# Optimization experiments

Measured on AMD Instinct MI355X. Metric: run time of the kernel, lower is better.

The kernel has to match this reference:

```python
import jax, jax.numpy as jnp
import numpy as np
import math

# SS2D (VMamba v2) config
D_MODEL = 96
D_INNER = 192          # ssm_ratio * d_model (== d_expand, ssm_rank_ratio==ssm_ratio)
D_STATE = 16
DT_RANK = 6            # ceil(96/16)
K = 4                  # scan directions
D_CONV = 3
STEP = 2               # EfficientScan step_size
BATCH, H, W = 4, 64, 64  # H,W chosen even -> no padding branch
LN_EPS = 1e-5


def efficient_scan(x):
    # x: (B, C, H, W) with H,W divisible by STEP -> (B, 4, C, (H/2)*(W/2))
    Bn, C = x.shape[0], x.shape[1]
    xt = jnp.swapaxes(x, 2, 3)  # (B, C, W, H)
    xs0 = x[:, :, ::STEP, ::STEP].reshape(Bn, C, -1)
    xs1 = xt[:, :, ::STEP, 1::STEP].reshape(Bn, C, -1)
    xs2 = x[:, :, ::STEP, 1::STEP].reshape(Bn, C, -1)
    xs3 = xt[:, :, 1::STEP, 1::STEP].reshape(Bn, C, -1)
    return jnp.stack([xs0, xs1, xs2, xs3], axis=1)


def efficient_merge(ys, ori_h, ori_w):
    # ys: (B, 4, C, L') -> (B, C, ori_h*ori_w)
    Bn, _, C, _ = ys.shape
    Hs, Ws = ori_h // STEP, ori_w // STEP
    a = ys[:, 0].reshape(Bn, C, Hs, Ws)
    b = jnp.swapaxes(ys[:, 1].reshape(Bn, C, Ws, Hs), 2, 3)
    c = ys[:, 2].reshape(Bn, C, Hs, Ws)
    d = jnp.swapaxes(ys[:, 3].reshape(Bn, C, Ws, Hs), 2, 3)
    y = jnp.zeros((Bn, C, ori_h, ori_w), ys.dtype)
    y = y.at[:, :, ::STEP, ::STEP].set(a)
    y = y.at[:, :, 1::STEP, ::STEP].set(b)
    y = y.at[:, :, ::STEP, 1::STEP].set(c)
    y = y.at[:, :, 1::STEP, 1::STEP].set(d)
    return y.reshape(Bn, C, ori_h * ori_w)


def selective_scan(u, delta, A, Bs, Cs, D, delta_bias):
    # u, delta: (B, K*Dg, L); A: (K*Dg, N); Bs, Cs: (B, K, N, L); D, delta_bias: (K*Dg,)
    Bn, KD, L = u.shape
    N = A.shape[1]
    Dg = KD // K
    delta = jax.nn.softplus(delta + delta_bias[None, :, None])
    u4 = u.reshape(Bn, K, Dg, L)
    dt4 = delta.reshape(Bn, K, Dg, L)
    A4 = A.reshape(K, Dg, N)
    # discretized transition / input, time-major for scan: (L, B, K, Dg, N)
    dA = jnp.exp(jnp.einsum('bkdl,kdn->lbkdn', dt4, A4))
    dBu = jnp.einsum('bkdl,bknl,bkdl->lbkdn', dt4, Bs, u4)

    def step(h, inp):
        dA_t, dBu_t = inp
        h = dA_t * h + dBu_t
        return h, h

    h0 = jnp.zeros((Bn, K, Dg, N), u.dtype)
    _, hs = jax.lax.scan(step, h0, (dA, dBu))  # (L, B, K, Dg, N)
    y = jnp.einsum('lbkdn,bknl->bkdl', hs, Cs)
    y = y + u4 * D.reshape(1, K, Dg, 1)
    return y.reshape(Bn, KD, L)


def setup_inputs() -> dict:
    key = jax.random.key(0)
    ks = jax.random.split(key, 10)
    f = jnp.float32
    x = jax.random.normal(ks[0], (BATCH, H, W, D_MODEL), f)
    W_in = jax.random.normal(ks[1], (2 * D_INNER, D_MODEL), f) / math.sqrt(D_MODEL)
    conv_w = jax.random.normal(ks[2], (D_INNER, 1, D_CONV, D_CONV), f) / math.sqrt(D_CONV * D_CONV)
    conv_b = jax.random.normal(ks[3], (D_INNER,), f) * 0.01
    x_proj_weight = jax.random.normal(ks[4], (K, DT_RANK + 2 * D_STATE, D_INNER), f) / math.sqrt(D_INNER)
    dt_projs_weight = jax.random.normal(ks[5], (K, D_INNER, DT_RANK), f) / math.sqrt(DT_RANK)
    dt_projs_bias = jax.random.normal(ks[6], (K, D_INNER), f) * 0.1
    A_logs = jnp.log(jnp.tile(jnp.arange(1, D_STATE + 1, dtype=f), (K * D_INNER, 1)))
    Ds = jnp.ones((K * D_INNER,), f)
    ln_g = jnp.ones((D_INNER,), f)
    ln_b = jnp.zeros((D_INNER,), f)
    W_out = jax.random.normal(ks[7], (D_MODEL, D_INNER), f) / math.sqrt(D_INNER)
    return dict(x=x, W_in=W_in, conv_w=conv_w, conv_b=conv_b,
                x_proj_weight=x_proj_weight, dt_projs_weight=dt_projs_weight,
                dt_projs_bias=dt_projs_bias, A_logs=A_logs, Ds=Ds,
                ln_g=ln_g, ln_b=ln_b, W_out=W_out)


def _ss2d_forward(x, W_in, conv_w, conv_b, x_proj_weight, dt_projs_weight,
                  dt_projs_bias, A_logs, Ds, ln_g, ln_b, W_out):
    Bn = x.shape[0]
    # in_proj (no bias), split into x and gate z
    xz = jnp.einsum('bhwc,ec->bhwe', x, W_in)            # (B,H,W,2*D_INNER)
    xin, z = jnp.split(xz, 2, axis=-1)
    z = jax.nn.silu(z)
    # depthwise conv 3x3 (SAME) + SiLU, NCHW
    xc = jnp.transpose(xin, (0, 3, 1, 2))                 # (B, D_INNER, H, W)
    xc = jax.lax.conv_general_dilated(
        xc, conv_w, window_strides=(1, 1), padding=((1, 1), (1, 1)),
        feature_group_count=D_INNER,
        dimension_numbers=('NCHW', 'OIHW', 'NCHW')) + conv_b[None, :, None, None]
    xc = jax.nn.silu(xc)
    # cross_selective_scan
    xs = efficient_scan(xc)                               # (B, 4, C, L')
    Lp = xs.shape[-1]
    x_dbl = jnp.einsum('bkdl,kcd->bkcl', xs, x_proj_weight)
    dts, Bs, Cs = jnp.split(x_dbl, [DT_RANK, DT_RANK + D_STATE], axis=2)
    dts = jnp.einsum('bkrl,kdr->bkdl', dts, dt_projs_weight)
    u = xs.reshape(Bn, -1, Lp).astype(jnp.float32)
    delta = dts.reshape(Bn, -1, Lp).astype(jnp.float32)
    A = -jnp.exp(A_logs.astype(jnp.float32))
    ys = selective_scan(u, delta, A, Bs.astype(jnp.float32), Cs.astype(jnp.float32),
                        Ds.astype(jnp.float32), dt_projs_bias.reshape(-1).astype(jnp.float32))
    ys = ys.reshape(Bn, K, -1, Lp)
    y = efficient_merge(ys, H, W)                         # (B, C, H*W)
    y = jnp.swapaxes(y, 1, 2)                             # (B, L, C)
    # LayerNorm over channel dim
    mu = jnp.mean(y, axis=-1, keepdims=True)
    var = jnp.var(y, axis=-1, keepdims=True)
    y = (y - mu) * jax.lax.rsqrt(var + LN_EPS) * ln_g + ln_b
    y = y.reshape(Bn, H, W, D_INNER).astype(x.dtype)
    # gate and out_proj (no bias)
    y = y * z
    out = jnp.einsum('bhwd,od->bhwo', y, W_out)
    return out


def reference(x, W_in, conv_w, conv_b, x_proj_weight, dt_projs_weight,
              dt_projs_bias, A_logs, Ds, ln_g, ln_b, W_out):
    return _ss2d_forward(x, W_in, conv_w, conv_b, x_proj_weight, dt_projs_weight,
                         dt_projs_bias, A_logs, Ds, ln_g, ln_b, W_out)
```

## Files before the change

### kernel.cpp

```cpp
#include <hip/hip_runtime.h>
#include <math.h>


#define DINNER 192
#define NSTATE 16
#define KDIR 4
#define BATCH 4
#define NPIX (BATCH * 64 * 64)
#define LP 1024
#define NCH 64
#define CHUNK 16
#define NBK (BATCH * KDIR)
#define NSTATES (NBK * DINNER * NSTATE)
#define SSTRIDE (NBK * DINNER)
#define USTRIDE 196
#define GSTRIDE 200

typedef __attribute__((ext_vector_type(8))) short short8;
typedef __attribute__((ext_vector_type(4))) short short4v;
typedef __attribute__((ext_vector_type(4))) float f32x4;

__device__ __forceinline__ float silu_f(float x) {
    return x / (1.0f + __expf(-x));
}
__device__ __forceinline__ float softplus_f(float a) {
    return (a > 20.0f) ? a : __logf(1.0f + __expf(a));
}
__device__ __forceinline__ unsigned short f2bf(float f) {
    unsigned u = __float_as_uint(f);
    unsigned r = (u + 0x7FFFu + ((u >> 16) & 1u)) >> 16;
    return (unsigned short)r;
}
__device__ __forceinline__ float bf2f(unsigned short h) {
    return __uint_as_float(((unsigned)h) << 16);
}

__global__ __launch_bounds__(256) void k_castW(
        const float* __restrict__ W_in, const float* __restrict__ W_out,
        unsigned short* __restrict__ Wi_hi, unsigned short* __restrict__ Wi_lo,
        unsigned short* __restrict__ Wo_bf) {
    int i = blockIdx.x * 256 + threadIdx.x;
    if (i < 384 * 96) {
        float v = W_in[i];
        unsigned short h = f2bf(v);
        Wi_hi[i] = h;
        Wi_lo[i] = f2bf(v - bf2f(h));
    }
    if (i < 96 * DINNER) Wo_bf[i] = f2bf(W_out[i]);
}

__global__ __launch_bounds__(256) void k_inproj3(
        const float* __restrict__ x,
        const unsigned short* __restrict__ Wi_hi,
        const unsigned short* __restrict__ Wi_lo,
        float* __restrict__ xin, float* __restrict__ z) {
    int p0 = blockIdx.x * 16;
    int w = threadIdx.x >> 6;
    int lane = threadIdx.x & 63;
    int m = lane & 15, quad = lane >> 4;
    const short* wh = (const short*)Wi_hi;
    const short* wl = (const short*)Wi_lo;
    short8 ah[3], al[3];
    #pragma unroll
    for (int c = 0; c < 3; ++c) {
        const float* xr = x + (size_t)(p0 + m) * 96 + c * 32 + quad * 8;
        short8 hi, lo;
        #pragma unroll
        for (int j = 0; j < 8; ++j) {
            float v = xr[j];
            unsigned short hb = f2bf(v);
            hi[j] = (short)hb;
            lo[j] = (short)f2bf(v - bf2f(hb));
        }
        ah[c] = hi;
        al[c] = lo;
    }
    #pragma unroll
    for (int i = 0; i < 6; ++i) {
        int e0 = (w * 6 + i) * 16;
        f32x4 acc = {0.f, 0.f, 0.f, 0.f};
        #pragma unroll
        for (int c = 0; c < 3; ++c) {
            size_t o = (size_t)(e0 + m) * 96 + c * 32 + quad * 8;
            short8 bh = *(const short8*)(wh + o);
            short8 bl = *(const short8*)(wl + o);
            acc = __builtin_amdgcn_mfma_f32_16x16x32_bf16(ah[c], bl, acc, 0, 0, 0);
            acc = __builtin_amdgcn_mfma_f32_16x16x32_bf16(al[c], bh, acc, 0, 0, 0);
            acc = __builtin_amdgcn_mfma_f32_16x16x32_bf16(ah[c], bh, acc, 0, 0, 0);
        }
        int e = e0 + m;
        #pragma unroll
        for (int r = 0; r < 4; ++r) {
            int p = p0 + quad * 4 + r;
            if (e < 192) xin[(size_t)p * 192 + e] = acc[r];
            else         z[(size_t)p * 192 + (e - 192)] = silu_f(acc[r]);
        }
    }
}

__global__ __launch_bounds__(192) void k_conv8(
        const float* __restrict__ xin, const float* __restrict__ cw,
        const float* __restrict__ cb, float* __restrict__ xg) {
    int blk = blockIdx.x;
    int b = blk >> 9;
    int rem = blk & 511;
    int h = rem >> 3;
    int w0 = (rem & 7) * 8;
    int d = threadIdx.x;
    float wr[3][3];
    #pragma unroll
    for (int i = 0; i < 3; ++i)
        #pragma unroll
        for (int j = 0; j < 3; ++j) wr[i][j] = cw[d * 9 + i * 3 + j];
    float bias = cb[d];
    float acc[8];
    #pragma unroll
    for (int o = 0; o < 8; ++o) acc[o] = bias;
    #pragma unroll
    for (int jj = 0; jj < 10; ++jj) {
        int ww = w0 + jj - 1;
        float r0 = 0.0f, r1 = 0.0f, r2 = 0.0f;
        if ((unsigned)ww < 64u) {
            const float* base = xin + ((size_t)b * 4096 + h * 64 + ww) * 192 + d;
            if (h > 0)  r0 = base[-64 * 192];
            r1 = base[0];
            if (h < 63) r2 = base[64 * 192];
        }
        #pragma unroll
        for (int dd2 = 0; dd2 < 3; ++dd2) {
            int o = jj - 2 + dd2;
            int cj = 2 - dd2;
            if (o >= 0 && o < 8) {
                acc[o] = fmaf(r0, wr[0][cj], acc[o]);
                acc[o] = fmaf(r1, wr[1][cj], acc[o]);
                acc[o] = fmaf(r2, wr[2][cj], acc[o]);
            }
        }
    }
    #pragma unroll
    for (int o = 0; o < 8; ++o) {
        int w = w0 + o;
        int kq = (h & 1) ? ((w & 1) ? 3 : 1) : ((w & 1) ? 2 : 0);
        int l = (kq & 1) ? ((w >> 1) * 32 + (h >> 1))
                         : ((h >> 1) * 32 + (w >> 1));
        xg[((size_t)(b * 4 + kq) * 1024 + l) * 192 + d] = silu_f(acc[o]);
    }
}

__global__ __launch_bounds__(192) void k_xdbl(
        const float* __restrict__ xg, const float* __restrict__ xpw,
        float* __restrict__ dtr, float* __restrict__ Bm, float* __restrict__ Cm) {
    __shared__ float sU[16 * USTRIDE];
    int bk = blockIdx.x >> 6;
    int tile = blockIdx.x & 63;
    int k = bk & 3;
    int t = threadIdx.x;
    int lbase = bk * 1024 + tile * 16;
    const float4* usrc = (const float4*)(xg + (size_t)lbase * 192);
    for (int i = t; i < 16 * 48; i += 192) {
        int l = i / 48, c4 = i - l * 48;
        *(float4*)&sU[l * USTRIDE + c4 * 4] = usrc[i];
    }
    __syncthreads();
    int l = t & 15, cgp = t >> 4;
    float acc[4] = {0.f, 0.f, 0.f, 0.f};
    int c3 = (cgp < 2) ? (cgp + 36) : cgp;
    const float* wb = xpw + (size_t)k * 38 * 192;
    for (int qv = 0; qv < 48; ++qv) {
        float4 xv = *(const float4*)&sU[l * USTRIDE + qv * 4];
        float4 w0 = *(const float4*)&wb[(cgp +  0) * 192 + qv * 4];
        float4 w1 = *(const float4*)&wb[(cgp + 12) * 192 + qv * 4];
        float4 w2 = *(const float4*)&wb[(cgp + 24) * 192 + qv * 4];
        float4 w3 = *(const float4*)&wb[(size_t)c3 * 192 + qv * 4];
        acc[0] = fmaf(xv.x, w0.x, fmaf(xv.y, w0.y, fmaf(xv.z, w0.z, fmaf(xv.w, w0.w, acc[0]))));
        acc[1] = fmaf(xv.x, w1.x, fmaf(xv.y, w1.y, fmaf(xv.z, w1.z, fmaf(xv.w, w1.w, acc[1]))));
        acc[2] = fmaf(xv.x, w2.x, fmaf(xv.y, w2.y, fmaf(xv.z, w2.z, fmaf(xv.w, w2.w, acc[2]))));
        acc[3] = fmaf(xv.x, w3.x, fmaf(xv.y, w3.y, fmaf(xv.z, w3.z, fmaf(xv.w, w3.w, acc[3]))));
    }
    int bkl = lbase + l;
    #pragma unroll
    for (int j = 0; j < 4; ++j) {
        int c = cgp + 12 * j;
        if (j == 3) { if (cgp >= 2) break; c = cgp + 36; }
        float v = acc[j];
        if (c < 6)       dtr[(size_t)bkl * 6 + c] = v;
        else if (c < 22) Bm[(size_t)bkl * 16 + (c - 6)] = v;
        else             Cm[(size_t)bkl * 16 + (c - 22)] = v;
    }
}

__global__ __launch_bounds__(192) void k_scan1p(
        const float* __restrict__ xg, const float* __restrict__ dtr,
        const float* __restrict__ Bm, const float* __restrict__ A_logs,
        const float* __restrict__ dtw, const float* __restrict__ dtb,
        float* __restrict__ Sbuf, float* __restrict__ Qbuf) {
    __shared__ float sU[CHUNK * USTRIDE];
    __shared__ float sB[CHUNK * 16];
    int bk = blockIdx.x >> 6;
    int ch = blockIdx.x & 63;
    int k = bk & 3;
    int d = threadIdx.x;
    int lbase = bk * 1024 + ch * CHUNK;
    const float4* usrc = (const float4*)(xg + (size_t)lbase * 192);
    for (int i = d; i < CHUNK * 48; i += 192) {
        int l = i / 48, c4 = i - l * 48;
        *(float4*)&sU[l * USTRIDE + c4 * 4] = usrc[i];
    }
    for (int i = d; i < CHUNK * 16; i += 192) sB[i] = Bm[(size_t)lbase * 16 + i];
    float A[16];
    #pragma unroll
    for (int n = 0; n < 16; ++n) A[n] = -__expf(A_logs[(k * 192 + d) * 16 + n]);
    float A0 = A[0];
    bool geo = true;
    #pragma unroll
    for (int n = 1; n < 16; ++n)
        geo = geo && (fabsf(A[n] - (float)(n + 1) * A0) <= 1e-4f * fabsf(A[n]));
    float wp[6];
    #pragma unroll
    for (int q = 0; q < 6; ++q) wp[q] = dtw[(k * 192 + d) * 6 + q];
    float bias = dtb[k * 192 + d];
    __syncthreads();
    float h[16];
    #pragma unroll
    for (int n = 0; n < 16; ++n) h[n] = 0.0f;
    float S = 0.0f;
    for (int l = 0; l < CHUNK; ++l) {
        const float* r = dtr + (size_t)(lbase + l) * 6;
        float a = bias;
        #pragma unroll
        for (int q = 0; q < 6; ++q) a = fmaf(wp[q], r[q], a);
        float dlt = softplus_f(a);
        S += dlt;
        float du = dlt * sU[l * USTRIDE + d];
        if (geo) {
            float e1 = __expf(dlt * A0);
            float e = e1;
            #pragma unroll
            for (int n = 0; n < 16; ++n) {
                h[n] = fmaf(e, h[n], du * sB[l * 16 + n]);
                e *= e1;
            }
        } else {
            #pragma unroll
            for (int n = 0; n < 16; ++n) {
                float e = __expf(dlt * A[n]);
                h[n] = fmaf(e, h[n], du * sB[l * 16 + n]);
            }
        }
    }
    Sbuf[(size_t)ch * SSTRIDE + bk * 192 + d] = S;
    size_t base = (size_t)ch * NSTATES + bk * (192 * 16);
    #pragma unroll
    for (int n = 0; n < 16; ++n)
        Qbuf[base + n * 192 + d] = h[n];
}

__global__ __launch_bounds__(256) void k_scan2(
        const float* __restrict__ Sbuf, const float* __restrict__ A_logs,
        float* QH) {
    int s = blockIdx.x * 256 + threadIdx.x;
    int bk = s / 3072;
    int rem = s - bk * 3072;
    int n = rem / 192;
    int d = rem - n * 192;
    int k = bk & 3;
    float A = -__expf(A_logs[(k * 192 + d) * 16 + n]);
    float h = 0.0f;
    for (int c = 0; c < NCH; ++c) {
        float q = QH[(size_t)c * NSTATES + s];
        float S = Sbuf[(size_t)c * SSTRIDE + bk * 192 + d];
        float p = __expf(A * S);
        QH[(size_t)c * NSTATES + s] = h;
        h = fmaf(p, h, q);
    }
}

__global__ __launch_bounds__(192) void k_scan3p(
        const float* __restrict__ xg, const float* __restrict__ dtr,
        const float* __restrict__ Bm, const float* __restrict__ Cm,
        const float* __restrict__ A_logs, const float* __restrict__ dtw,
        const float* __restrict__ dtb, const float* __restrict__ Ds,
        const float* __restrict__ QH, float* __restrict__ yout) {
    __shared__ float sU[CHUNK * USTRIDE];
    __shared__ float sB[CHUNK * 16];
    __shared__ float sC[CHUNK * 16];
    int bk = blockIdx.x >> 6;
    int ch = blockIdx.x & 63;
    int k = bk & 3;
    int d = threadIdx.x;
    int lbase = bk * 1024 + ch * CHUNK;
    const float4* usrc = (const float4*)(xg + (size_t)lbase * 192);
    for (int i = d; i < CHUNK * 48; i += 192) {
        int l = i / 48, c4 = i - l * 48;
        *(float4*)&sU[l * USTRIDE + c4 * 4] = usrc[i];
    }
    for (int i = d; i < CHUNK * 16; i += 192) {
        sB[i] = Bm[(size_t)lbase * 16 + i];
        sC[i] = Cm[(size_t)lbase * 16 + i];
    }
    float A[16];
    #pragma unroll
    for (int n = 0; n < 16; ++n) A[n] = -__expf(A_logs[(k * 192 + d) * 16 + n]);
    float A0 = A[0];
    bool geo = true;
    #pragma unroll
    for (int n = 1; n < 16; ++n)
        geo = geo && (fabsf(A[n] - (float)(n + 1) * A0) <= 1e-4f * fabsf(A[n]));
    float wp[6];
    #pragma unroll
    for (int q = 0; q < 6; ++q) wp[q] = dtw[(k * 192 + d) * 6 + q];
    float bias = dtb[k * 192 + d];
    float Dp = Ds[k * 192 + d];
    float h[16];
    size_t base = (size_t)ch * NSTATES + bk * (192 * 16);
    #pragma unroll
    for (int n = 0; n < 16; ++n) h[n] = QH[base + n * 192 + d];
    __syncthreads();
    for (int l = 0; l < CHUNK; ++l) {
        const float* r = dtr + (size_t)(lbase + l) * 6;
        float a = bias;
        #pragma unroll
        for (int q = 0; q < 6; ++q) a = fmaf(wp[q], r[q], a);
        float dlt = softplus_f(a);
        float u = sU[l * USTRIDE + d];
        float du = dlt * u;
        float y = 0.0f;
        if (geo) {
            float e1 = __expf(dlt * A0);
            float e = e1;
            #pragma unroll
            for (int n = 0; n < 16; ++n) {
                h[n] = fmaf(e, h[n], du * sB[l * 16 + n]);
                y = fmaf(h[n], sC[l * 16 + n], y);
                e *= e1;
            }
        } else {
            #pragma unroll
            for (int n = 0; n < 16; ++n) {
                float e = __expf(dlt * A[n]);
                h[n] = fmaf(e, h[n], du * sB[l * 16 + n]);
                y = fmaf(h[n], sC[l * 16 + n], y);
            }
        }
        yout[(size_t)(lbase + l) * 192 + d] = fmaf(u, Dp, y);
    }
}

__global__ __launch_bounds__(256) void k_lnout(
        const float* __restrict__ yout, const float* __restrict__ z,
        const float* __restrict__ lng, const float* __restrict__ lnb,
        const unsigned short* __restrict__ Wo_bf, float* __restrict__ out) {
    __shared__ __align__(16) short sgb[32 * GSTRIDE];
    int p0 = blockIdx.x * 32;
    int t = threadIdx.x;
    int p = t >> 3;
    int sub = t & 7;
    int gp = p0 + p;
    int b = gp >> 12;
    int hw = gp & 4095;
    int h = hw >> 6, w = hw & 63;
    int kq = (h & 1) ? ((w & 1) ? 3 : 1) : ((w & 1) ? 2 : 0);
    int l = (kq & 1) ? ((w >> 1) * 32 + (h >> 1))
                     : ((h >> 1) * 32 + (w >> 1));
    const float* yrow = yout + ((size_t)(b * 4 + kq) * 1024 + l) * 192 + sub * 24;
    float4 yv[6];
    float s = 0.0f, s2 = 0.0f;
    #pragma unroll
    for (int j = 0; j < 6; ++j) {
        float4 v = *(const float4*)(yrow + j * 4);
        yv[j] = v;
        s += v.x + v.y + v.z + v.w;
        s2 += v.x * v.x + v.y * v.y + v.z * v.z + v.w * v.w;
    }
    #pragma unroll
    for (int off = 1; off < 8; off <<= 1) {
        s  += __shfl_xor(s, off, 8);
        s2 += __shfl_xor(s2, off, 8);
    }
    float mu = s * (1.0f / 192.0f);
    float var = s2 * (1.0f / 192.0f) - mu * mu;
    float rstd = rsqrtf(var + 1e-5f);
    const float* zrow = z + (size_t)gp * 192 + sub * 24;
    short* grow = sgb + p * GSTRIDE + sub * 24;
    #pragma unroll
    for (int j = 0; j < 6; ++j) {
        float4 zv = *(const float4*)(zrow + j * 4);
        float4 gv = *(const float4*)(lng + sub * 24 + j * 4);
        float4 bv = *(const float4*)(lnb + sub * 24 + j * 4);
        short4v sv;
        sv.x = (short)f2bf(((yv[j].x - mu) * rstd * gv.x + bv.x) * zv.x);
        sv.y = (short)f2bf(((yv[j].y - mu) * rstd * gv.y + bv.y) * zv.y);
        sv.z = (short)f2bf(((yv[j].z - mu) * rstd * gv.z + bv.z) * zv.z);
        sv.w = (short)f2bf(((yv[j].w - mu) * rstd * gv.w + bv.w) * zv.w);
        *(short4v*)(grow + j * 4) = sv;
    }
    __syncthreads();
    int wv = t >> 6;
    int lane = t & 63;
    int m = lane & 15, quad = lane >> 4;
    int mt = wv >> 1;
    int nb = (wv & 1) * 3;
    const short* wob = (const short*)Wo_bf;
    short8 a[6];
    #pragma unroll
    for (int kk = 0; kk < 6; ++kk)
        a[kk] = *(const short8*)(sgb + (mt * 16 + m) * GSTRIDE + kk * 32 + quad * 8);
    #pragma unroll
    for (int i = 0; i < 3; ++i) {
        int n0 = (nb + i) * 16;
        f32x4 acc = {0.f, 0.f, 0.f, 0.f};
        #pragma unroll
        for (int kk = 0; kk < 6; ++kk) {
            short8 bfr = *(const short8*)(wob + (size_t)(n0 + m) * 192 + kk * 32 + quad * 8);
            acc = __builtin_amdgcn_mfma_f32_16x16x32_bf16(a[kk], bfr, acc, 0, 0, 0);
        }
        #pragma unroll
        for (int r = 0; r < 4; ++r) {
            int pp = p0 + mt * 16 + quad * 4 + r;
            out[(size_t)pp * 96 + n0 + m] = acc[r];
        }
    }
}

extern "C" void kernel_launch(void* const* d_in, const int* in_sizes, int n_in,
                              void* d_out, int out_size, void* d_ws, size_t ws_size,
                              hipStream_t stream) {
    const float* x    = (const float*)d_in[0];
    const float* W_in = (const float*)d_in[1];
    const float* cw   = (const float*)d_in[2];
    const float* cb   = (const float*)d_in[3];
    const float* xpw  = (const float*)d_in[4];
    const float* dtw  = (const float*)d_in[5];
    const float* dtb  = (const float*)d_in[6];
    const float* Alog = (const float*)d_in[7];
    const float* Ds   = (const float*)d_in[8];
    const float* lng  = (const float*)d_in[9];
    const float* lnb  = (const float*)d_in[10];
    const float* Wout = (const float*)d_in[11];
    float* out = (float*)d_out;

    float* ws = (float*)d_ws;
    size_t off = 0;
    unsigned short* Wi_hi = (unsigned short*)(ws + off); off += 384 * 96 / 2;
    unsigned short* Wi_lo = (unsigned short*)(ws + off); off += 384 * 96 / 2;
    unsigned short* Wo_bf = (unsigned short*)(ws + off); off += 96 * DINNER / 2;
    float* xin   = ws + off; off += (size_t)NPIX * 192;
    float* zbuf  = ws + off; off += (size_t)NPIX * 192;
    float* xg    = ws + off; off += (size_t)NPIX * 192;
    float* dtrb  = ws + off; off += (size_t)NBK * LP * 6;
    float* Bm    = ws + off; off += (size_t)NBK * LP * 16;
    float* Cm    = ws + off; off += (size_t)NBK * LP * 16;
    float* Sbuf  = ws + off; off += (size_t)NCH * SSTRIDE;
    float* QH    = ws + off; off += (size_t)NCH * NSTATES;
    float* yout  = ws + off; off += (size_t)NBK * LP * 192;

    hipLaunchKernelGGL(k_castW, dim3(144), dim3(256), 0, stream,
                       W_in, Wout, Wi_hi, Wi_lo, Wo_bf);
    hipLaunchKernelGGL(k_inproj3, dim3(NPIX / 16), dim3(256), 0, stream,
                       x, Wi_hi, Wi_lo, xin, zbuf);
    hipLaunchKernelGGL(k_conv8, dim3(NPIX / 8), dim3(192), 0, stream,
                       xin, cw, cb, xg);
    hipLaunchKernelGGL(k_xdbl, dim3(NBK * 64), dim3(192), 0, stream,
                       xg, xpw, dtrb, Bm, Cm);
    hipLaunchKernelGGL(k_scan1p, dim3(NBK * NCH), dim3(192), 0, stream,
                       xg, dtrb, Bm, Alog, dtw, dtb, Sbuf, QH);
    hipLaunchKernelGGL(k_scan2, dim3(NSTATES / 256), dim3(256), 0, stream,
                       Sbuf, Alog, QH);
    hipLaunchKernelGGL(k_scan3p, dim3(NBK * NCH), dim3(192), 0, stream,
                       xg, dtrb, Bm, Cm, Alog, dtw, dtb, Ds, QH, yout);
    hipLaunchKernelGGL(k_lnout, dim3(NPIX / 32), dim3(256), 0, stream,
                       yout, zbuf, lng, lnb, Wo_bf, out);
}
```

Baseline: 174.0 us.

## Compute local scan output in first pass, add carry-in correction in third pass

The first chunked-scan kernel now emits each chunk's output from a zero initial state as well as its end state and delta sum. The third pass no longer reruns the full recurrence. Instead it adds the carry-in term, the starting state decayed by exp(A*cumulative delta) and contracted with C, and it skips chunk 0 entirely. This removes the second full recurrence and the reloads of u and B. In exchange yout is read and written an extra time and the decay exponent is recomputed from a running sum.

```diff
diff --git a/kernel.cpp b/kernel.cpp
--- a/kernel.cpp
+++ b/kernel.cpp
@@ -189,98 +189,13 @@
     }
 }
 
-__global__ __launch_bounds__(192) void k_scan1p(
-        const float* __restrict__ xg, const float* __restrict__ dtr,
-        const float* __restrict__ Bm, const float* __restrict__ A_logs,
-        const float* __restrict__ dtw, const float* __restrict__ dtb,
-        float* __restrict__ Sbuf, float* __restrict__ Qbuf) {
-    __shared__ float sU[CHUNK * USTRIDE];
-    __shared__ float sB[CHUNK * 16];
-    int bk = blockIdx.x >> 6;
-    int ch = blockIdx.x & 63;
-    int k = bk & 3;
-    int d = threadIdx.x;
-    int lbase = bk * 1024 + ch * CHUNK;
-    const float4* usrc = (const float4*)(xg + (size_t)lbase * 192);
-    for (int i = d; i < CHUNK * 48; i += 192) {
-        int l = i / 48, c4 = i - l * 48;
-        *(float4*)&sU[l * USTRIDE + c4 * 4] = usrc[i];
-    }
-    for (int i = d; i < CHUNK * 16; i += 192) sB[i] = Bm[(size_t)lbase * 16 + i];
-    float A[16];
-    #pragma unroll
-    for (int n = 0; n < 16; ++n) A[n] = -__expf(A_logs[(k * 192 + d) * 16 + n]);
-    float A0 = A[0];
-    bool geo = true;
-    #pragma unroll
-    for (int n = 1; n < 16; ++n)
-        geo = geo && (fabsf(A[n] - (float)(n + 1) * A0) <= 1e-4f * fabsf(A[n]));
-    float wp[6];
-    #pragma unroll
-    for (int q = 0; q < 6; ++q) wp[q] = dtw[(k * 192 + d) * 6 + q];
-    float bias = dtb[k * 192 + d];
-    __syncthreads();
-    float h[16];
-    #pragma unroll
-    for (int n = 0; n < 16; ++n) h[n] = 0.0f;
-    float S = 0.0f;
-    for (int l = 0; l < CHUNK; ++l) {
-        const float* r = dtr + (size_t)(lbase + l) * 6;
-        float a = bias;
-        #pragma unroll
-        for (int q = 0; q < 6; ++q) a = fmaf(wp[q], r[q], a);
-        float dlt = softplus_f(a);
-        S += dlt;
-        float du = dlt * sU[l * USTRIDE + d];
-        if (geo) {
-            float e1 = __expf(dlt * A0);
-            float e = e1;
-            #pragma unroll
-            for (int n = 0; n < 16; ++n) {
-                h[n] = fmaf(e, h[n], du * sB[l * 16 + n]);
-                e *= e1;
-            }
-        } else {
-            #pragma unroll
-            for (int n = 0; n < 16; ++n) {
-                float e = __expf(dlt * A[n]);
-                h[n] = fmaf(e, h[n], du * sB[l * 16 + n]);
-            }
-        }
-    }
-    Sbuf[(size_t)ch * SSTRIDE + bk * 192 + d] = S;
-    size_t base = (size_t)ch * NSTATES + bk * (192 * 16);
-    #pragma unroll
-    for (int n = 0; n < 16; ++n)
-        Qbuf[base + n * 192 + d] = h[n];
-}
-
-__global__ __launch_bounds__(256) void k_scan2(
-        const float* __restrict__ Sbuf, const float* __restrict__ A_logs,
-        float* QH) {
-    int s = blockIdx.x * 256 + threadIdx.x;
-    int bk = s / 3072;
-    int rem = s - bk * 3072;
-    int n = rem / 192;
-    int d = rem - n * 192;
-    int k = bk & 3;
-    float A = -__expf(A_logs[(k * 192 + d) * 16 + n]);
-    float h = 0.0f;
-    for (int c = 0; c < NCH; ++c) {
-        float q = QH[(size_t)c * NSTATES + s];
-        float S = Sbuf[(size_t)c * SSTRIDE + bk * 192 + d];
-        float p = __expf(A * S);
-        QH[(size_t)c * NSTATES + s] = h;
-        h = fmaf(p, h, q);
-    }
-}
-
-__global__ __launch_bounds__(192) void k_scan3p(
+__global__ __launch_bounds__(192) void k_scan1y(
         const float* __restrict__ xg, const float* __restrict__ dtr,
         const float* __restrict__ Bm, const float* __restrict__ Cm,
         const float* __restrict__ A_logs, const float* __restrict__ dtw,
         const float* __restrict__ dtb, const float* __restrict__ Ds,
-        const float* __restrict__ QH, float* __restrict__ yout) {
+        float* __restrict__ Sbuf, float* __restrict__ Qbuf,
+        float* __restrict__ yout) {
     __shared__ float sU[CHUNK * USTRIDE];
     __shared__ float sB[CHUNK * 16];
     __shared__ float sC[CHUNK * 16];
@@ -311,17 +226,18 @@
     for (int q = 0; q < 6; ++q) wp[q] = dtw[(k * 192 + d) * 6 + q];
     float bias = dtb[k * 192 + d];
     float Dp = Ds[k * 192 + d];
+    __syncthreads();
     float h[16];
-    size_t base = (size_t)ch * NSTATES + bk * (192 * 16);
-    #pragma unroll
-    for (int n = 0; n < 16; ++n) h[n] = QH[base + n * 192 + d];
-    __syncthreads();
+    #pragma unroll
+    for (int n = 0; n < 16; ++n) h[n] = 0.0f;
+    float S = 0.0f;
     for (int l = 0; l < CHUNK; ++l) {
         const float* r = dtr + (size_t)(lbase + l) * 6;
         float a = bias;
         #pragma unroll
         for (int q = 0; q < 6; ++q) a = fmaf(wp[q], r[q], a);
         float dlt = softplus_f(a);
+        S += dlt;
         float u = sU[l * USTRIDE + d];
         float du = dlt * u;
         float y = 0.0f;
@@ -344,6 +260,90 @@
         }
         yout[(size_t)(lbase + l) * 192 + d] = fmaf(u, Dp, y);
     }
+    Sbuf[(size_t)ch * SSTRIDE + bk * 192 + d] = S;
+    size_t base = (size_t)ch * NSTATES + bk * (192 * 16);
+    #pragma unroll
+    for (int n = 0; n < 16; ++n)
+        Qbuf[base + n * 192 + d] = h[n];
+}
+
+__global__ __launch_bounds__(256) void k_scan2(
+        const float* __restrict__ Sbuf, const float* __restrict__ A_logs,
+        float* QH) {
+    int s = blockIdx.x * 256 + threadIdx.x;
+    int bk = s / 3072;
+    int rem = s - bk * 3072;
+    int n = rem / 192;
+    int d = rem - n * 192;
+    int k = bk & 3;
+    float A = -__expf(A_logs[(k * 192 + d) * 16 + n]);
+    float h = 0.0f;
+    for (int c = 0; c < NCH; ++c) {
+        float q = QH[(size_t)c * NSTATES + s];
+        float S = Sbuf[(size_t)c * SSTRIDE + bk * 192 + d];
+        float p = __expf(A * S);
+        QH[(size_t)c * NSTATES + s] = h;
+        h = fmaf(p, h, q);
+    }
+}
+
+__global__ __launch_bounds__(192) void k_scan3c(
+        const float* __restrict__ dtr, const float* __restrict__ Cm,
+        const float* __restrict__ A_logs, const float* __restrict__ dtw,
+        const float* __restrict__ dtb, const float* __restrict__ QH,
+        float* __restrict__ yout) {
+    __shared__ float sC[CHUNK * 16];
+    int bk = blockIdx.x >> 6;
+    int ch = blockIdx.x & 63;
+    if (ch == 0) return;
+    int k = bk & 3;
+    int d = threadIdx.x;
+    int lbase = bk * 1024 + ch * CHUNK;
+    for (int i = d; i < CHUNK * 16; i += 192)
+        sC[i] = Cm[(size_t)lbase * 16 + i];
+    float A[16];
+    #pragma unroll
+    for (int n = 0; n < 16; ++n) A[n] = -__expf(A_logs[(k * 192 + d) * 16 + n]);
+    float A0 = A[0];
+    bool geo = true;
+    #pragma unroll
+    for (int n = 1; n < 16; ++n)
+        geo = geo && (fabsf(A[n] - (float)(n + 1) * A0) <= 1e-4f * fabsf(A[n]));
+    float wp[6];
+    #pragma unroll
+    for (int q = 0; q < 6; ++q) wp[q] = dtw[(k * 192 + d) * 6 + q];
+    float bias = dtb[k * 192 + d];
+    float h0[16];
+    size_t base = (size_t)ch * NSTATES + bk * (192 * 16);
+    #pragma unroll
+    for (int n = 0; n < 16; ++n) h0[n] = QH[base + n * 192 + d];
+    __syncthreads();
+    float S = 0.0f;
+    for (int l = 0; l < CHUNK; ++l) {
+        const float* r = dtr + (size_t)(lbase + l) * 6;
+        float a = bias;
+        #pragma unroll
+        for (int q = 0; q < 6; ++q) a = fmaf(wp[q], r[q], a);
+        S += softplus_f(a);
+        float y = yout[(size_t)(lbase + l) * 192 + d];
+        float corr = 0.0f;
+        if (geo) {
+            float e1 = __expf(A0 * S);
+            float e = e1;
+            #pragma unroll
+            for (int n = 0; n < 16; ++n) {
+                corr = fmaf(h0[n] * e, sC[l * 16 + n], corr);
+                e *= e1;
+            }
+        } else {
+            #pragma unroll
+            for (int n = 0; n < 16; ++n) {
+                float e = __expf(A[n] * S);
+                corr = fmaf(h0[n] * e, sC[l * 16 + n], corr);
+            }
+        }
+        yout[(size_t)(lbase + l) * 192 + d] = y + corr;
+    }
 }
 
 __global__ __launch_bounds__(256) void k_lnout(
@@ -462,12 +462,12 @@
                        xin, cw, cb, xg);
     hipLaunchKernelGGL(k_xdbl, dim3(NBK * 64), dim3(192), 0, stream,
                        xg, xpw, dtrb, Bm, Cm);
-    hipLaunchKernelGGL(k_scan1p, dim3(NBK * NCH), dim3(192), 0, stream,
-                       xg, dtrb, Bm, Alog, dtw, dtb, Sbuf, QH);
+    hipLaunchKernelGGL(k_scan1y, dim3(NBK * NCH), dim3(192), 0, stream,
+                       xg, dtrb, Bm, Cm, Alog, dtw, dtb, Ds, Sbuf, QH, yout);
     hipLaunchKernelGGL(k_scan2, dim3(NSTATES / 256), dim3(256), 0, stream,
                        Sbuf, Alog, QH);
-    hipLaunchKernelGGL(k_scan3p, dim3(NBK * NCH), dim3(192), 0, stream,
-                       xg, dtrb, Bm, Cm, Alog, dtw, dtb, Ds, QH, yout);
+    hipLaunchKernelGGL(k_scan3c, dim3(NBK * NCH), dim3(192), 0, stream,
+                       dtrb, Cm, Alog, dtw, dtb, QH, yout);
     hipLaunchKernelGGL(k_lnout, dim3(NPIX / 32), dim3(256), 0, stream,
                        yout, zbuf, lng, lnb, Wo_bf, out);
 }
```

Result: no change. 174.6 us (+0.4%).
